# Optimization experiments

Hardware: AMD Instinct MI355X
Metric: run time of the kernel (lower is better)

## Reference

```python
import jax, jax.numpy as jnp
import numpy as np

R_ROT = 6   # rotation order R
r = 7       # icosahedral resolution
H, W = 2 ** r, 2 ** (r + 1)


def _reorder_idx(r, R):
    """Flat gather indices implementing FlatPadIco boundary stitching."""
    H, W = 2 ** r, 2 ** (r + 1)
    idx_in = np.arange(R * 5 * H * W, dtype=np.int64).reshape(R, 5, H, W)
    idx_out = np.zeros((R, 5, H + 2, W + 2), dtype=np.int64)
    idx_out[..., 1:-1, 1:-1] = idx_in
    idx_out[..., 0, 1:2 ** r + 1] = np.roll(idx_in, 1, -3)[..., -1, 2 ** r:]
    idx_out[..., 0, 2 ** r + 1:-1] = np.roll(np.roll(idx_in, 1, -3), -1, -4)[..., :, -1][..., ::-1]
    idx_out[..., -1, 2:2 ** r + 2] = np.roll(np.roll(idx_in, -1, -3), -1, -4)[..., :, 0][..., ::-1]
    idx_out[..., -1, 2 ** r + 1:-1] = np.roll(idx_in, -1, -3)[..., 0, 0:2 ** r]
    idx_out[..., 1:-1, 0] = np.roll(np.roll(idx_in, 1, -3), 1, -4)[..., -1, 0:2 ** r][..., ::-1]
    idx_out[..., 2:, -1] = np.roll(np.roll(idx_in, -1, -3), 1, -4)[..., 0, 2 ** r:][..., ::-1]
    return idx_out


def _neighbor_idx(r):
    """7-neighbor (hex) indices into the padded (H+2, W+2) charts."""
    dh = np.array([0, 1, 1, 0, -1, -1, 0], dtype=np.int64)
    dw = np.array([0, 0, 1, 1, 0, -1, -1], dtype=np.int64)
    h = np.arange(2 ** (r - 1), dtype=np.int64)
    w = np.arange(2 ** r, dtype=np.int64)
    nh = 1 + 2 * h[:, None, None] + dh[None, None, :]   # (H/2, 1, 7)
    nw = 1 + 2 * w[None, :, None] + dw[None, None, :]   # (1, W/2, 7)
    shape = (2 ** (r - 1), 2 ** r, 7)
    return np.broadcast_to(nh, shape).copy(), np.broadcast_to(nw, shape).copy()


def _clean_mask(rr):
    """CleanVertices mask: zero the two pole pixels of each chart."""
    m = np.ones((2 ** rr, 2 ** (rr + 1)), dtype=np.float32)
    m[-1, 0] = 0.0   # north pole vertex
    m[0, -1] = 0.0   # south pole vertex
    return m


_RIDX = jnp.asarray(_reorder_idx(r, R_ROT))
_NH, _NW = (jnp.asarray(a) for a in _neighbor_idx(r))
_MASK_IN = jnp.asarray(_clean_mask(r))
_MASK_OUT = jnp.asarray(_clean_mask(r - 1))


def setup_inputs() -> dict:
    key = jax.random.key(0)
    x = jax.random.normal(key, (4, 16, R_ROT, 5, H, W), dtype=jnp.float32)
    return {"x": x}


def reference(x) -> jnp.ndarray:
    # CleanVertices(r) inside FlatPadIco
    x = x * _MASK_IN
    # FlatPadIco: flatten (R, charts, H, W) and gather with stitched indices
    xf = x.reshape(x.shape[:-4] + (-1,))          # (..., R*5*H*W)
    y = xf[..., _RIDX]                            # (..., R, 5, H+2, W+2)
    # 7-neighbor gather + mean pooling
    rf = y[..., _NH, _NW]                         # (..., R, 5, H/2, W/2, 7)
    out = jnp.mean(rf, axis=-1)                   # (..., R, 5, H/2, W/2)
    # CleanVertices(r-1) on pooled output
    return out * _MASK_OUT
```

## Files before the change

### kernel.cpp

```cpp
#include <hip/hip_runtime.h>


#define WW 256

typedef float vfloat4 __attribute__((ext_vector_type(4)));

__global__ __launch_bounds__(256) void flat_pool_ico(const float* __restrict__ x,
                                                     float* __restrict__ out) {
    int t = blockIdx.x * 256 + threadIdx.x;
    int lane = t & 15;
    int rowid = t >> 4;
    int h = rowid & 63;
    int tmp = rowid >> 6;
    int c = tmp % 5; tmp /= 5;
    int rot = tmp % 6;
    int b = tmp / 6;
    int w0 = lane << 3;
    int cm = w0 << 1;

    long slab = (long)((b * 6 + rot) * 5 + c);
    const float* xs   = x + (slab << 15);
    const float* rowm = xs + (h << 9);
    const float* rowb = rowm + WW;

    float M[17], T[16], B[16];

    {
        vfloat4 a0 = *(const vfloat4*)(rowm + cm);
        vfloat4 a1 = *(const vfloat4*)(rowm + cm + 4);
        vfloat4 a2 = *(const vfloat4*)(rowm + cm + 8);
        vfloat4 a3 = *(const vfloat4*)(rowm + cm + 12);
        M[1]=a0.x;  M[2]=a0.y;  M[3]=a0.z;  M[4]=a0.w;
        M[5]=a1.x;  M[6]=a1.y;  M[7]=a1.z;  M[8]=a1.w;
        M[9]=a2.x;  M[10]=a2.y; M[11]=a2.z; M[12]=a2.w;
        M[13]=a3.x; M[14]=a3.y; M[15]=a3.z; M[16]=a3.w;
        vfloat4 c0 = *(const vfloat4*)(rowb + cm);
        vfloat4 c1 = *(const vfloat4*)(rowb + cm + 4);
        vfloat4 c2 = *(const vfloat4*)(rowb + cm + 8);
        vfloat4 c3 = *(const vfloat4*)(rowb + cm + 12);
        B[0]=c0.x;  B[1]=c0.y;  B[2]=c0.z;  B[3]=c0.w;
        B[4]=c1.x;  B[5]=c1.y;  B[6]=c1.z;  B[7]=c1.w;
        B[8]=c2.x;  B[9]=c2.y;  B[10]=c2.z; B[11]=c2.w;
        B[12]=c3.x; B[13]=c3.y; B[14]=c3.z; B[15]=c3.w;
    }

    int cprev = (c + 4) % 5;
    const float* xn3 = x + ((long)((b * 6 + (rot + 5) % 6) * 5 + cprev) << 15) + 127 * WW;

    {
        float midL = __shfl_up(M[16], 1);
        if (lane == 0) midL = xn3[127 - (h << 1)];
        M[0] = midL;
    }

    if (h == 0) {
        const float* xn1 = x + ((long)((b * 6 + rot) * 5 + cprev) << 15) + 127 * WW + 127;
        const float* xn2 = x + ((long)((b * 6 + (rot + 1) % 6) * 5 + cprev) << 15) + 255;
        #pragma unroll
        for (int i = 0; i < 16; ++i) {
            int pw = cm + i;
            float v;
            if (pw == 0)        v = x[(long)b * 983040];
            else if (pw <= 128) v = xn1[pw];
            else                v = xn2[(256 - pw) << 8];
            T[i] = v;
        }
    } else {
        const float* rowt = rowm - WW;
        vfloat4 t0 = *(const vfloat4*)(rowt + cm);
        vfloat4 t1 = *(const vfloat4*)(rowt + cm + 4);
        vfloat4 t2 = *(const vfloat4*)(rowt + cm + 8);
        vfloat4 t3 = *(const vfloat4*)(rowt + cm + 12);
        T[1]=t0.x;  T[2]=t0.y;  T[3]=t0.z;  T[4]=t0.w;
        T[5]=t1.x;  T[6]=t1.y;  T[7]=t1.z;  T[8]=t1.w;
        T[9]=t2.x;  T[10]=t2.y; T[11]=t2.z; T[12]=t2.w;
        T[13]=t3.x; T[14]=t3.y; T[15]=t3.z;
        float topL = __shfl_up(t3.w, 1);
        if (lane == 0) topL = xn3[128 - (h << 1)];
        T[0] = topL;
    }

    const float inv7 = 1.0f / 7.0f;
    float o[8];
    #pragma unroll
    for (int k = 0; k < 8; ++k) {
        float s = M[2*k] + M[2*k+1] + M[2*k+2]
                + T[2*k] + T[2*k+1]
                + B[2*k] + B[2*k+1];
        o[k] = s * inv7;
    }

    if (h == 63 && lane == 0)  o[0] = 0.0f;
    if (h == 0  && lane == 15) o[7] = 0.0f;

    float* op = out + (slab << 13) + (h << 7) + w0;
    vfloat4 s0 = { o[0], o[1], o[2], o[3] };
    vfloat4 s1 = { o[4], o[5], o[6], o[7] };
    __builtin_nontemporal_store(s0, (vfloat4*)op);
    __builtin_nontemporal_store(s1, (vfloat4*)(op + 4));
}

extern "C" void kernel_launch(void* const* d_in, const int* in_sizes, int n_in,
                              void* d_out, int out_size, void* d_ws, size_t ws_size,
                              hipStream_t stream) {
    const float* x = (const float*)d_in[0];
    float* out = (float*)d_out;
    flat_pool_ico<<<7680, 256, 0, stream>>>(x, out);
}
```

Baseline: 58.79 us.

## Process four output rows per thread and reuse bottom row as next top

Each block now handles one whole chart slab, and each thread computes four consecutive pooled rows. The bottom input row of one step is shifted into the top-row registers for the next, which avoids reloading shared top rows. This reduces redundant global and L2 reads and index arithmetic. In exchange the grid is four times smaller and each thread's loads are serialized across rows, which may reduce memory-level parallelism.

```diff
diff --git a/kernel.cpp b/kernel.cpp
--- a/kernel.cpp
+++ b/kernel.cpp
@@ -5,56 +5,45 @@
 
 typedef float vfloat4 __attribute__((ext_vector_type(4)));
 
+__device__ __forceinline__ void load16(const float* p, float* d) {
+    vfloat4 a = *(const vfloat4*)(p);
+    vfloat4 b = *(const vfloat4*)(p + 4);
+    vfloat4 c = *(const vfloat4*)(p + 8);
+    vfloat4 e = *(const vfloat4*)(p + 12);
+    d[0]=a.x;  d[1]=a.y;  d[2]=a.z;  d[3]=a.w;
+    d[4]=b.x;  d[5]=b.y;  d[6]=b.z;  d[7]=b.w;
+    d[8]=c.x;  d[9]=c.y;  d[10]=c.z; d[11]=c.w;
+    d[12]=e.x; d[13]=e.y; d[14]=e.z; d[15]=e.w;
+}
+
 __global__ __launch_bounds__(256) void flat_pool_ico(const float* __restrict__ x,
                                                      float* __restrict__ out) {
-    int t = blockIdx.x * 256 + threadIdx.x;
-    int lane = t & 15;
-    int rowid = t >> 4;
-    int h = rowid & 63;
-    int tmp = rowid >> 6;
-    int c = tmp % 5; tmp /= 5;
-    int rot = tmp % 6;
-    int b = tmp / 6;
-    int w0 = lane << 3;
-    int cm = w0 << 1;
+    int slab = blockIdx.x;
+    int lane = threadIdx.x & 15;
+    int hb   = (threadIdx.x >> 4) << 2;
+    int c    = slab % 5;
+    int rc   = slab / 5;
+    int rot  = rc % 6;
+    int b    = rc / 6;
+    int cm   = lane << 4;
 
-    long slab = (long)((b * 6 + rot) * 5 + c);
-    const float* xs   = x + (slab << 15);
-    const float* rowm = xs + (h << 9);
-    const float* rowb = rowm + WW;
-
-    float M[17], T[16], B[16];
-
-    {
-        vfloat4 a0 = *(const vfloat4*)(rowm + cm);
-        vfloat4 a1 = *(const vfloat4*)(rowm + cm + 4);
-        vfloat4 a2 = *(const vfloat4*)(rowm + cm + 8);
-        vfloat4 a3 = *(const vfloat4*)(rowm + cm + 12);
-        M[1]=a0.x;  M[2]=a0.y;  M[3]=a0.z;  M[4]=a0.w;
-        M[5]=a1.x;  M[6]=a1.y;  M[7]=a1.z;  M[8]=a1.w;
-        M[9]=a2.x;  M[10]=a2.y; M[11]=a2.z; M[12]=a2.w;
-        M[13]=a3.x; M[14]=a3.y; M[15]=a3.z; M[16]=a3.w;
-        vfloat4 c0 = *(const vfloat4*)(rowb + cm);
-        vfloat4 c1 = *(const vfloat4*)(rowb + cm + 4);
-        vfloat4 c2 = *(const vfloat4*)(rowb + cm + 8);
-        vfloat4 c3 = *(const vfloat4*)(rowb + cm + 12);
-        B[0]=c0.x;  B[1]=c0.y;  B[2]=c0.z;  B[3]=c0.w;
-        B[4]=c1.x;  B[5]=c1.y;  B[6]=c1.z;  B[7]=c1.w;
-        B[8]=c2.x;  B[9]=c2.y;  B[10]=c2.z; B[11]=c2.w;
-        B[12]=c3.x; B[13]=c3.y; B[14]=c3.z; B[15]=c3.w;
-    }
-
+    const float* xs = x + ((long)slab << 15);
     int cprev = (c + 4) % 5;
     const float* xn3 = x + ((long)((b * 6 + (rot + 5) % 6) * 5 + cprev) << 15) + 127 * WW;
 
+    float T[16], M[17], B[16];
+
+    const float* rowm = xs + (hb << 9);
+    load16(rowm + cm, &M[1]);
     {
-        float midL = __shfl_up(M[16], 1);
-        if (lane == 0) midL = xn3[127 - (h << 1)];
-        M[0] = midL;
+        float ml = __shfl_up(M[16], 1);
+        if (lane == 0) ml = xn3[127 - (hb << 1)];
+        M[0] = ml;
     }
+    load16(rowm + WW + cm, B);
 
-    if (h == 0) {
-        const float* xn1 = x + ((long)((b * 6 + rot) * 5 + cprev) << 15) + 127 * WW + 127;
+    if (hb == 0) {
+        const float* xn1 = x + ((long)(rc * 5 + cprev) << 15) + 127 * WW + 127;
         const float* xn2 = x + ((long)((b * 6 + (rot + 1) % 6) * 5 + cprev) << 15) + 255;
         #pragma unroll
         for (int i = 0; i < 16; ++i) {
@@ -66,38 +55,51 @@
             T[i] = v;
         }
     } else {
-        const float* rowt = rowm - WW;
-        vfloat4 t0 = *(const vfloat4*)(rowt + cm);
-        vfloat4 t1 = *(const vfloat4*)(rowt + cm + 4);
-        vfloat4 t2 = *(const vfloat4*)(rowt + cm + 8);
-        vfloat4 t3 = *(const vfloat4*)(rowt + cm + 12);
-        T[1]=t0.x;  T[2]=t0.y;  T[3]=t0.z;  T[4]=t0.w;
-        T[5]=t1.x;  T[6]=t1.y;  T[7]=t1.z;  T[8]=t1.w;
-        T[9]=t2.x;  T[10]=t2.y; T[11]=t2.z; T[12]=t2.w;
-        T[13]=t3.x; T[14]=t3.y; T[15]=t3.z;
-        float topL = __shfl_up(t3.w, 1);
-        if (lane == 0) topL = xn3[128 - (h << 1)];
-        T[0] = topL;
+        float tt[16];
+        load16(rowm - WW + cm, tt);
+        #pragma unroll
+        for (int i = 0; i < 15; ++i) T[i + 1] = tt[i];
+        float tl = __shfl_up(tt[15], 1);
+        if (lane == 0) tl = xn3[128 - (hb << 1)];
+        T[0] = tl;
     }
 
     const float inv7 = 1.0f / 7.0f;
-    float o[8];
+    float* op = out + ((long)slab << 13) + (hb << 7) + (lane << 3);
+
     #pragma unroll
-    for (int k = 0; k < 8; ++k) {
-        float s = M[2*k] + M[2*k+1] + M[2*k+2]
-                + T[2*k] + T[2*k+1]
-                + B[2*k] + B[2*k+1];
-        o[k] = s * inv7;
+    for (int hh = 0; hh < 4; ++hh) {
+        int h = hb + hh;
+        float o[8];
+        #pragma unroll
+        for (int k = 0; k < 8; ++k) {
+            float s = M[2*k] + M[2*k+1] + M[2*k+2]
+                    + T[2*k] + T[2*k+1]
+                    + B[2*k] + B[2*k+1];
+            o[k] = s * inv7;
+        }
+        if (h == 63 && lane == 0)  o[0] = 0.0f;
+        if (h == 0  && lane == 15) o[7] = 0.0f;
+
+        vfloat4 s0 = { o[0], o[1], o[2], o[3] };
+        vfloat4 s1 = { o[4], o[5], o[6], o[7] };
+        __builtin_nontemporal_store(s0, (vfloat4*)(op + (hh << 7)));
+        __builtin_nontemporal_store(s1, (vfloat4*)(op + (hh << 7) + 4));
+
+        if (hh < 3) {
+            float tl = __shfl_up(B[15], 1);
+            if (lane == 0) tl = xn3[128 - ((h + 1) << 1)];
+            #pragma unroll
+            for (int j = 15; j >= 1; --j) T[j] = B[j - 1];
+            T[0] = tl;
+            const float* rm = xs + ((h + 1) << 9);
+            load16(rm + cm, &M[1]);
+            float ml = __shfl_up(M[16], 1);
+            if (lane == 0) ml = xn3[127 - ((h + 1) << 1)];
+            M[0] = ml;
+            load16(rm + WW + cm, B);
+        }
     }
-
-    if (h == 63 && lane == 0)  o[0] = 0.0f;
-    if (h == 0  && lane == 15) o[7] = 0.0f;
-
-    float* op = out + (slab << 13) + (h << 7) + w0;
-    vfloat4 s0 = { o[0], o[1], o[2], o[3] };
-    vfloat4 s1 = { o[4], o[5], o[6], o[7] };
-    __builtin_nontemporal_store(s0, (vfloat4*)op);
-    __builtin_nontemporal_store(s1, (vfloat4*)(op + 4));
 }
 
 extern "C" void kernel_launch(void* const* d_in, const int* in_sizes, int n_in,
@@ -105,5 +107,5 @@
                               hipStream_t stream) {
     const float* x = (const float*)d_in[0];
     float* out = (float*)d_out;
-    flat_pool_ico<<<7680, 256, 0, stream>>>(x, out);
+    flat_pool_ico<<<1920, 256, 0, stream>>>(x, out);
 }
```

After: 68.76 us. 17.0% more time.
